# Optimization experiments

Measured on AMD Instinct MI355X. Metric: run time of the kernel, lower is better.

The kernel has to match this reference:

```python
import jax, jax.numpy as jnp
import numpy as np

N_NODES = 100000
N_EDGES = 1600000
IN_FEATS = 256
OUT_DIM = 128


def setup_inputs() -> dict:
    key = jax.random.key(0)
    k_x, k_e, k_w = jax.random.split(key, 3)
    x = jax.random.normal(k_x, (N_NODES, IN_FEATS), dtype=jnp.float32)
    edge_index = jax.random.randint(k_e, (2, N_EDGES), 0, N_NODES, dtype=jnp.int64)
    # Glorot-ish init for the GCN weight
    W = jax.random.normal(k_w, (IN_FEATS, OUT_DIM), dtype=jnp.float32) * (1.0 / np.sqrt(IN_FEATS))
    b = jnp.zeros((OUT_DIM,), dtype=jnp.float32)
    return {"x": x, "edge_index": edge_index, "W": W, "b": b}


def reference(x, edge_index, W, b):
    N = x.shape[0]
    # GCN with self-loops and symmetric normalization (PyG gcn_norm)
    self_loops = jnp.arange(N, dtype=edge_index.dtype)
    row = jnp.concatenate([edge_index[0], self_loops])  # source nodes
    col = jnp.concatenate([edge_index[1], self_loops])  # target nodes
    deg = jnp.zeros((N,), dtype=x.dtype).at[col].add(1.0)
    deg_inv_sqrt = jnp.where(deg > 0, jax.lax.rsqrt(jnp.maximum(deg, 1.0)), 0.0)
    norm = deg_inv_sqrt[row] * deg_inv_sqrt[col]  # [E+N]
    # Linear transform first (small GEMM), then sparse aggregation
    h = x @ W + b                                  # [N, out_dim]
    msg = h[row] * norm[:, None]                   # gather + scale, [E+N, out_dim]
    out = jax.ops.segment_sum(msg, col, num_segments=N)  # scatter-add
    # relu; dropout is identity in eval mode
    return jax.nn.relu(out)
```

## Files before the change

### kernel.cpp

```cpp
#include <hip/hip_runtime.h>

typedef __attribute__((ext_vector_type(8))) short short8;
typedef __attribute__((ext_vector_type(4))) float f32x4;

#define IN_F 256
#define OUT_F 128
#define NPB 256
#define MAXCAP 5120

__device__ __forceinline__ float bf2f(unsigned int u16) {
    union { unsigned int i; float f; } v; v.i = u16 << 16; return v.f;
}
__device__ __forceinline__ unsigned short f2bf(float f) {
    union { float f; unsigned int i; } v; v.f = f;
    unsigned int u = v.i;
    return (unsigned short)((u + 0x7fffu + ((u >> 16) & 1u)) >> 16);
}

__global__ __launch_bounds__(256) void k_bin(const int* __restrict__ row, const int* __restrict__ col,
                                             int* __restrict__ bcur, int* __restrict__ ebuf,
                                             int E, int NBr, int chunk) {
    __shared__ int hist[512];
    __shared__ int cbase[512];
    int t = threadIdx.x;
    int e0 = blockIdx.x * chunk;
    int e1 = e0 + chunk; if (e1 > E) e1 = E;

    for (int i = t; i < NBr; i += 256) hist[i] = 0;
    __syncthreads();
    for (int i = e0 + t; i < e1; i += 256)
        atomicAdd(&hist[col[i] >> 8], 1);
    __syncthreads();
    for (int i = t; i < NBr; i += 256) {
        int h = hist[i];
        cbase[i] = h ? atomicAdd(&bcur[i], h) : 0;
    }
    __syncthreads();
    for (int i = t; i < NBr; i += 256) hist[i] = 0;
    __syncthreads();
    for (int i = e0 + t; i < e1; i += 256) {
        int c = col[i];
        int r = row[i];
        int b = c >> 8;
        int p = atomicAdd(&hist[b], 1) + cbase[b];
        ebuf[(size_t)b * MAXCAP + p] = (r << 8) | (c & 255);
    }
}

__global__ __launch_bounds__(256) void k_fine(const int* __restrict__ bcur, const int* __restrict__ ebuf,
                                              int* __restrict__ offs, int* __restrict__ deg,
                                              float* __restrict__ dis, int* __restrict__ srci, int N) {
    __shared__ int dl[256];
    __shared__ int sc[256];
    int b = blockIdx.x;
    int t = threadIdx.x;
    int count = bcur[b];
    const int* eb = ebuf + (size_t)b * MAXCAP;

    dl[t] = 0;
    __syncthreads();
    for (int i = t; i < count; i += 256)
        atomicAdd(&dl[eb[i] & 255], 1);
    __syncthreads();
    int myDeg = dl[t];
    sc[t] = myDeg; __syncthreads();
    for (int off = 1; off < 256; off <<= 1) {
        int a = (t >= off) ? sc[t - off] : 0;
        __syncthreads();
        sc[t] += a;
        __syncthreads();
    }
    int excl = sc[t] - myDeg;
    int node = (b << 8) + t;
    int bbase = b * MAXCAP;
    if (node < N) {
        offs[node] = bbase + excl;
        deg[node] = myDeg;
        dis[node] = rsqrtf((float)myDeg + 1.0f);
    }
    dl[t] = excl;
    __syncthreads();
    for (int i = t; i < count; i += 256) {
        int p = eb[i];
        int pos = atomicAdd(&dl[p & 255], 1);
        srci[bbase + pos] = p >> 8;
    }
}

__global__ __launch_bounds__(256) void k_transposeW(const float* __restrict__ W,
                                                    unsigned short* __restrict__ Wt,
                                                    unsigned short* __restrict__ hb, int N) {
    int idx = blockIdx.x * 256 + threadIdx.x;
    if (idx < IN_F * OUT_F) {
        int k = idx >> 7;
        int n = idx & 127;
        Wt[n * IN_F + k] = f2bf(W[idx]);
    }
    if (idx < OUT_F) hb[(size_t)N * OUT_F + idx] = 0;
}

__global__ __launch_bounds__(256) void k_gemm(const float* __restrict__ x,
                                              const unsigned short* __restrict__ Wt,
                                              const float* __restrict__ bias,
                                              const float* __restrict__ dis,
                                              unsigned short* __restrict__ hb, int nrows) {
    int wave = threadIdx.x >> 6;
    int lane = threadIdx.x & 63;
    int m = lane & 15;
    int quad = lane >> 4;

    int row0 = blockIdx.x * 128 + wave * 32;
    int nm1 = nrows - 1;
    int rA = row0 + m;      if (rA > nm1) rA = nm1;
    int rB = row0 + 16 + m; if (rB > nm1) rB = nm1;

    const float4* pa = (const float4*)(x + (size_t)rA * IN_F) + 2 * quad;
    const float4* pb = (const float4*)(x + (size_t)rB * IN_F) + 2 * quad;
    const short8* wf = (const short8*)Wt + (size_t)m * 32 + quad;

    f32x4 acc[2][8];
#pragma unroll
    for (int t = 0; t < 2; t++)
#pragma unroll
        for (int ct = 0; ct < 8; ct++) acc[t][ct] = (f32x4){0.f, 0.f, 0.f, 0.f};

    float4 a0 = pa[0], a1 = pa[1];
    float4 b0 = pb[0], b1 = pb[1];
    short8 w[8];
#pragma unroll
    for (int ct = 0; ct < 8; ct++) w[ct] = wf[ct * 512];

#pragma unroll
    for (int i = 0; i < 8; i++) {
        float4 na0 = {}, na1 = {}, nb0 = {}, nb1 = {};
        short8 nw[8] = {};
        if (i < 7) {
            na0 = pa[8 * (i + 1)];     na1 = pa[8 * (i + 1) + 1];
            nb0 = pb[8 * (i + 1)];     nb1 = pb[8 * (i + 1) + 1];
#pragma unroll
            for (int ct = 0; ct < 8; ct++) nw[ct] = wf[ct * 512 + 4 * (i + 1)];
        }
        short8 af, bf;
        af[0] = (short)f2bf(a0.x); af[1] = (short)f2bf(a0.y);
        af[2] = (short)f2bf(a0.z); af[3] = (short)f2bf(a0.w);
        af[4] = (short)f2bf(a1.x); af[5] = (short)f2bf(a1.y);
        af[6] = (short)f2bf(a1.z); af[7] = (short)f2bf(a1.w);
        bf[0] = (short)f2bf(b0.x); bf[1] = (short)f2bf(b0.y);
        bf[2] = (short)f2bf(b0.z); bf[3] = (short)f2bf(b0.w);
        bf[4] = (short)f2bf(b1.x); bf[5] = (short)f2bf(b1.y);
        bf[6] = (short)f2bf(b1.z); bf[7] = (short)f2bf(b1.w);
#pragma unroll
        for (int ct = 0; ct < 8; ct++)
            acc[0][ct] = __builtin_amdgcn_mfma_f32_16x16x32_bf16(af, w[ct], acc[0][ct], 0, 0, 0);
#pragma unroll
        for (int ct = 0; ct < 8; ct++)
            acc[1][ct] = __builtin_amdgcn_mfma_f32_16x16x32_bf16(bf, w[ct], acc[1][ct], 0, 0, 0);
        a0 = na0; a1 = na1; b0 = nb0; b1 = nb1;
#pragma unroll
        for (int ct = 0; ct < 8; ct++) w[ct] = nw[ct];
    }

    float bv[8];
#pragma unroll
    for (int ct = 0; ct < 8; ct++) bv[ct] = bias[ct * 16 + m];

    int orow0 = blockIdx.x * 128 + wave * 32 + quad * 4;
#pragma unroll
    for (int t = 0; t < 2; t++) {
#pragma unroll
        for (int r = 0; r < 4; r++) {
            int orow = orow0 + t * 16 + r;
            if (orow < nrows) {
                float dr = dis[orow];
#pragma unroll
                for (int ct = 0; ct < 8; ct++)
                    hb[(size_t)orow * OUT_F + ct * 16 + m] = f2bf((acc[t][ct][r] + bv[ct]) * dr);
            }
        }
    }
}

__global__ __launch_bounds__(256) void k_agg(const unsigned short* __restrict__ hb,
                                             const float* __restrict__ dis,
                                             const int* __restrict__ offs, const int* __restrict__ deg,
                                             const int* __restrict__ srci,
                                             float* __restrict__ out, int n) {
    int node = blockIdx.x * 4 + (threadIdx.x >> 6);
    if (node >= n) return;
    int lane = threadIdx.x & 63;

    unsigned int v = *(const unsigned int*)(hb + (size_t)node * OUT_F + lane * 2);
    float ax = bf2f(v & 0xffffu);
    float ay = bf2f(v >> 16);

    int start = offs[node];
    int cnt = deg[node];

    for (int base = 0; base < cnt; base += 64) {
        int mm = cnt - base; if (mm > 64) mm = 64;
        int e = (lane < mm) ? srci[start + base + lane] : n;
        int mround = (mm + 7) & ~7;
        for (int j = 0; j < mround; j += 8) {
            int rr[8];
#pragma unroll
            for (int k = 0; k < 8; k++) rr[k] = __shfl(e, j + k);
            unsigned int w[8];
#pragma unroll
            for (int k = 0; k < 8; k++)
                w[k] = *(const unsigned int*)(hb + (size_t)rr[k] * OUT_F + lane * 2);
#pragma unroll
            for (int k = 0; k < 8; k++) {
                ax += bf2f(w[k] & 0xffffu);
                ay += bf2f(w[k] >> 16);
            }
        }
    }

    float di = dis[node];
    float2 o;
    o.x = fmaxf(ax * di, 0.f);
    o.y = fmaxf(ay * di, 0.f);
    *(float2*)(out + (size_t)node * OUT_F + lane * 2) = o;
}

static inline size_t alignup(size_t v, size_t a) { return (v + a - 1) & ~(a - 1); }

extern "C" void kernel_launch(void* const* d_in, const int* in_sizes, int n_in,
                              void* d_out, int out_size, void* d_ws, size_t ws_size,
                              hipStream_t stream) {
    const float* x  = (const float*)d_in[0];
    const int* ei   = (const int*)d_in[1];
    const float* W  = (const float*)d_in[2];
    const float* b  = (const float*)d_in[3];
    float* out      = (float*)d_out;

    const int N = in_sizes[0] / IN_F;
    const int E = in_sizes[1] / 2;
    const int* rowp = ei;
    const int* colp = ei + E;

    const int NBr = (N + NPB - 1) / NPB;

    char* ws = (char*)d_ws;
    size_t off = 0;
    int*   bcur   = (int*)(ws + off);   off = alignup(off + (size_t)NBr * 4, 256);
    int*   deg    = (int*)(ws + off);   off = alignup(off + (size_t)N * 4, 256);
    float* dis    = (float*)(ws + off); off = alignup(off + (size_t)N * 4, 256);
    int*   offs   = (int*)(ws + off);   off = alignup(off + (size_t)N * 4, 256);
    unsigned short* Wt = (unsigned short*)(ws + off); off = alignup(off + (size_t)IN_F * OUT_F * 2, 256);
    int*   ebuf   = (int*)(ws + off);   off = alignup(off + (size_t)NBr * MAXCAP * 4, 256);
    int*   srci   = (int*)(ws + off);   off = alignup(off + (size_t)NBr * MAXCAP * 4, 256);
    unsigned short* hb = (unsigned short*)(ws + off); off = alignup(off + (size_t)(N + 1) * OUT_F * 2, 256);

    (void)hipMemsetAsync(bcur, 0, (size_t)NBr * 4, stream);

    int chunk = (E + 511) / 512;
    k_bin<<<512, 256, 0, stream>>>(rowp, colp, bcur, ebuf, E, NBr, chunk);
    k_fine<<<NBr, 256, 0, stream>>>(bcur, ebuf, offs, deg, dis, srci, N);

    k_transposeW<<<(IN_F * OUT_F + 255) / 256, 256, 0, stream>>>(W, Wt, hb, N);
    k_gemm<<<(N + 127) / 128, 256, 0, stream>>>(x, Wt, b, dis, hb, N);

    k_agg<<<(N + 3) / 4, 256, 0, stream>>>(hb, dis, offs, deg, srci, out, N);
}
```

Measured before the change: 313.2 us.

## Stage pre-swizzled W in LDS via direct global-to-LDS loads in GEMM

The transposed bf16 weight is now written in an MFMA-fragment-ordered layout. Each GEMM block copies all of W (64 KB) into shared memory with global_load_lds, then reads weight fragments from LDS. Each wave now handles 16 rows instead of 32, and the whole x row slice is loaded into registers up front. Blocks cover 64 rows, which doubles the grid. The aim is to replace repeated global/L2 weight reads with LDS reads and to get more parallelism. The cost is that each block reloads the full 64 KB of W into LDS and gets less reuse per wave, and the large LDS footprint may limit occupancy.

After: 295.0 us. -5.8%, faster.

```diff
diff --git a/kernel.cpp b/kernel.cpp
--- a/kernel.cpp
+++ b/kernel.cpp
@@ -2,18 +2,19 @@
 
 typedef __attribute__((ext_vector_type(8))) short short8;
 typedef __attribute__((ext_vector_type(4))) float f32x4;
+typedef unsigned int u32;
 
 #define IN_F 256
 #define OUT_F 128
 #define NPB 256
 #define MAXCAP 5120
 
-__device__ __forceinline__ float bf2f(unsigned int u16) {
-    union { unsigned int i; float f; } v; v.i = u16 << 16; return v.f;
+__device__ __forceinline__ float bf2f(u32 u16) {
+    union { u32 i; float f; } v; v.i = u16 << 16; return v.f;
 }
 __device__ __forceinline__ unsigned short f2bf(float f) {
-    union { float f; unsigned int i; } v; v.f = f;
-    unsigned int u = v.i;
+    union { float f; u32 i; } v; v.f = f;
+    u32 u = v.i;
     return (unsigned short)((u + 0x7fffu + ((u >> 16) & 1u)) >> 16);
 }
 
@@ -94,7 +95,10 @@
     if (idx < IN_F * OUT_F) {
         int k = idx >> 7;
         int n = idx & 127;
-        Wt[n * IN_F + k] = f2bf(W[idx]);
+        int ct = n >> 4, mm = n & 15;
+        int i = k >> 5, q = (k >> 3) & 3, e = k & 7;
+        int d = (ct * 8 + i) * 64 + q * 16 + mm;
+        Wt[(size_t)d * 8 + e] = f2bf(W[idx]);
     }
     if (idx < OUT_F) hb[(size_t)N * OUT_F + idx] = 0;
 }
@@ -104,78 +108,71 @@
                                               const float* __restrict__ bias,
                                               const float* __restrict__ dis,
                                               unsigned short* __restrict__ hb, int nrows) {
+    __shared__ short8 WB[4096];
     int wave = threadIdx.x >> 6;
     int lane = threadIdx.x & 63;
     int m = lane & 15;
     int quad = lane >> 4;
 
-    int row0 = blockIdx.x * 128 + wave * 32;
+    int row0 = blockIdx.x * 64 + wave * 16;
     int nm1 = nrows - 1;
-    int rA = row0 + m;      if (rA > nm1) rA = nm1;
-    int rB = row0 + 16 + m; if (rB > nm1) rB = nm1;
-
-    const float4* pa = (const float4*)(x + (size_t)rA * IN_F) + 2 * quad;
-    const float4* pb = (const float4*)(x + (size_t)rB * IN_F) + 2 * quad;
-    const short8* wf = (const short8*)Wt + (size_t)m * 32 + quad;
-
-    f32x4 acc[2][8];
-#pragma unroll
-    for (int t = 0; t < 2; t++)
-#pragma unroll
-        for (int ct = 0; ct < 8; ct++) acc[t][ct] = (f32x4){0.f, 0.f, 0.f, 0.f};
-
-    float4 a0 = pa[0], a1 = pa[1];
-    float4 b0 = pb[0], b1 = pb[1];
-    short8 w[8];
-#pragma unroll
-    for (int ct = 0; ct < 8; ct++) w[ct] = wf[ct * 512];
-
+    int r = row0 + m; if (r > nm1) r = nm1;
+    const float4* px = (const float4*)(x + (size_t)r * IN_F);
+
+    float4 xa[16];
 #pragma unroll
     for (int i = 0; i < 8; i++) {
-        float4 na0 = {}, na1 = {}, nb0 = {}, nb1 = {};
-        short8 nw[8] = {};
-        if (i < 7) {
-            na0 = pa[8 * (i + 1)];     na1 = pa[8 * (i + 1) + 1];
-            nb0 = pb[8 * (i + 1)];     nb1 = pb[8 * (i + 1) + 1];
-#pragma unroll
-            for (int ct = 0; ct < 8; ct++) nw[ct] = wf[ct * 512 + 4 * (i + 1)];
-        }
-        short8 af, bf;
+        xa[2 * i]     = px[8 * i + 2 * quad];
+        xa[2 * i + 1] = px[8 * i + 2 * quad + 1];
+    }
+
+    {
+        const char* gb = (const char*)Wt;
+        char* lb = (char*)WB;
+#pragma unroll
+        for (int s = 0; s < 16; s++) {
+            int d = (wave * 16 + s) * 64;
+            __builtin_amdgcn_global_load_lds(
+                (const __attribute__((address_space(1))) u32*)(gb + (size_t)(d + lane) * 16),
+                (__attribute__((address_space(3))) u32*)(lb + (size_t)d * 16),
+                16, 0, 0);
+        }
+    }
+
+    float bv[8];
+#pragma unroll
+    for (int ct = 0; ct < 8; ct++) bv[ct] = bias[ct * 16 + m];
+
+    __syncthreads();
+
+    f32x4 acc[8];
+#pragma unroll
+    for (int ct = 0; ct < 8; ct++) acc[ct] = (f32x4){0.f, 0.f, 0.f, 0.f};
+
+#pragma unroll
+    for (int i = 0; i < 8; i++) {
+        float4 a0 = xa[2 * i], a1 = xa[2 * i + 1];
+        short8 af;
         af[0] = (short)f2bf(a0.x); af[1] = (short)f2bf(a0.y);
         af[2] = (short)f2bf(a0.z); af[3] = (short)f2bf(a0.w);
         af[4] = (short)f2bf(a1.x); af[5] = (short)f2bf(a1.y);
         af[6] = (short)f2bf(a1.z); af[7] = (short)f2bf(a1.w);
-        bf[0] = (short)f2bf(b0.x); bf[1] = (short)f2bf(b0.y);
-        bf[2] = (short)f2bf(b0.z); bf[3] = (short)f2bf(b0.w);
-        bf[4] = (short)f2bf(b1.x); bf[5] = (short)f2bf(b1.y);
-        bf[6] = (short)f2bf(b1.z); bf[7] = (short)f2bf(b1.w);
-#pragma unroll
-        for (int ct = 0; ct < 8; ct++)
-            acc[0][ct] = __builtin_amdgcn_mfma_f32_16x16x32_bf16(af, w[ct], acc[0][ct], 0, 0, 0);
-#pragma unroll
-        for (int ct = 0; ct < 8; ct++)
-            acc[1][ct] = __builtin_amdgcn_mfma_f32_16x16x32_bf16(bf, w[ct], acc[1][ct], 0, 0, 0);
-        a0 = na0; a1 = na1; b0 = nb0; b1 = nb1;
-#pragma unroll
-        for (int ct = 0; ct < 8; ct++) w[ct] = nw[ct];
-    }
-
-    float bv[8];
-#pragma unroll
-    for (int ct = 0; ct < 8; ct++) bv[ct] = bias[ct * 16 + m];
-
-    int orow0 = blockIdx.x * 128 + wave * 32 + quad * 4;
-#pragma unroll
-    for (int t = 0; t < 2; t++) {
-#pragma unroll
-        for (int r = 0; r < 4; r++) {
-            int orow = orow0 + t * 16 + r;
-            if (orow < nrows) {
-                float dr = dis[orow];
-#pragma unroll
-                for (int ct = 0; ct < 8; ct++)
-                    hb[(size_t)orow * OUT_F + ct * 16 + m] = f2bf((acc[t][ct][r] + bv[ct]) * dr);
-            }
+#pragma unroll
+        for (int ct = 0; ct < 8; ct++) {
+            short8 w = WB[ct * 512 + i * 64 + lane];
+            acc[ct] = __builtin_amdgcn_mfma_f32_16x16x32_bf16(af, w, acc[ct], 0, 0, 0);
+        }
+    }
+
+    int orow0 = row0 + quad * 4;
+#pragma unroll
+    for (int rr = 0; rr < 4; rr++) {
+        int orow = orow0 + rr;
+        if (orow < nrows) {
+            float dr = dis[orow];
+#pragma unroll
+            for (int ct = 0; ct < 8; ct++)
+                hb[(size_t)orow * OUT_F + ct * 16 + m] = f2bf((acc[ct][rr] + bv[ct]) * dr);
         }
     }
 }
@@ -259,7 +256,7 @@
     k_fine<<<NBr, 256, 0, stream>>>(bcur, ebuf, offs, deg, dis, srci, N);
 
     k_transposeW<<<(IN_F * OUT_F + 255) / 256, 256, 0, stream>>>(W, Wt, hb, N);
-    k_gemm<<<(N + 127) / 128, 256, 0, stream>>>(x, Wt, b, dis, hb, N);
+    k_gemm<<<(N + 63) / 64, 256, 0, stream>>>(x, Wt, b, dis, hb, N);
 
     k_agg<<<(N + 3) / 4, 256, 0, stream>>>(hb, dis, offs, deg, srci, out, N);
 }
```
